# Kernel tuning notes

Hardware: AMD Instinct MI355X
Metric: run time of the kernel (lower is better)

Reference implementation:

```python
import jax, jax.numpy as jnp
import numpy as np
from jax import lax

B, T_TOK, H, T_MEL, K = 32, 1024, 256, 4096, 5


def setup_inputs() -> dict:
    key = jax.random.key(0)
    ks = jax.random.split(key, 16)
    x = jax.random.normal(ks[0], (B, T_TOK, H), jnp.float32)
    token_nums = jax.random.randint(ks[1], (B,), T_TOK // 2, T_TOK)
    # ground-truth per-token durations in mel frames (avg ~4 frames/token)
    mels_alignations = jax.random.uniform(ks[2], (B, T_TOK), jnp.float32) * 8.0
    mels_gt_num = jax.random.randint(ks[3], (B,), T_MEL // 2, T_MEL)
    s = 1.0 / np.sqrt(H * K)
    conv1_w = jax.random.uniform(ks[4], (H, H, K), jnp.float32, -s, s)
    conv1_b = jax.random.uniform(ks[5], (H,), jnp.float32, -s, s)
    ln1_g = jnp.ones((H,), jnp.float32)
    ln1_b = jnp.zeros((H,), jnp.float32)
    conv2_w = jax.random.uniform(ks[6], (H, H, K), jnp.float32, -s, s)
    conv2_b = jax.random.uniform(ks[7], (H,), jnp.float32, -s, s)
    ln2_g = jnp.ones((H,), jnp.float32)
    ln2_b = jnp.zeros((H,), jnp.float32)
    sl = 1.0 / np.sqrt(H)
    lin_w = jax.random.uniform(ks[8], (1, H), jnp.float32, -sl, sl)
    lin_b = jax.random.uniform(ks[9], (1,), jnp.float32, -sl, sl)
    return {"x": x, "token_nums": token_nums, "mels_alignations": mels_alignations,
            "mels_gt_num": mels_gt_num, "conv1_w": conv1_w, "conv1_b": conv1_b,
            "ln1_g": ln1_g, "ln1_b": ln1_b, "conv2_w": conv2_w, "conv2_b": conv2_b,
            "ln2_g": ln2_g, "ln2_b": ln2_b, "lin_w": lin_w, "lin_b": lin_b}


def conv1d_same(x, w, b):
    # x: [B, T, H] -> conv over T with kernel [H_out, H_in, K], padding SAME
    y = lax.conv_general_dilated(x.transpose(0, 2, 1), w, (1,), 'SAME',
                                 dimension_numbers=('NCH', 'OIH', 'NCH'))
    return y.transpose(0, 2, 1) + b


def layer_norm(x, g, b, eps=1e-5):
    mu = jnp.mean(x, axis=-1, keepdims=True)
    var = jnp.mean(jnp.square(x - mu), axis=-1, keepdims=True)
    return (x - mu) * lax.rsqrt(var + eps) * g + b


def reference(x, token_nums, mels_alignations, mels_gt_num,
              conv1_w, conv1_b, ln1_g, ln1_b,
              conv2_w, conv2_b, ln2_g, ln2_b, lin_w, lin_b):
    # NOTE: original forward computes the conv1/ln1/relu1 branch then overwrites
    # m with conv2(x) -- the conv1 branch does not affect outputs, so it is skipped.
    m = conv1d_same(x, conv2_w, conv2_b)                 # [B, T_TOK, H]
    m = jax.nn.relu(layer_norm(m, ln2_g, ln2_b))
    m = (m @ lin_w.T + lin_b)[..., 0]                    # [B, T_TOK]
    mask = jnp.arange(T_TOK)[None, :] < token_nums[:, None]
    m = jnp.where(mask, m, 0.0)                          # mels_alignations_predicted
    exp_m = jnp.where(mask, jnp.exp(m), 0.0)
    mels_num_predicted = exp_m.sum(axis=1).astype(jnp.int32)

    # expansion: running-clipped cumsum of gt durations -> frame->token map
    cum = jnp.minimum(jnp.cumsum(mels_alignations, axis=1),
                      mels_gt_num[:, None].astype(jnp.float32))  # [B, T_TOK]
    frames = jnp.arange(T_MEL, dtype=jnp.float32)
    tok = jax.vmap(lambda c: jnp.searchsorted(c, frames, side='right'))(cum)  # [B, T_MEL]
    valid = tok < T_TOK
    tok_c = jnp.minimum(tok, T_TOK - 1)
    x_new = jnp.where(valid[:, :, None],
                      jnp.take_along_axis(x, tok_c[:, :, None], axis=1), 0.0)
    return x_new, m, mels_num_predicted
```

## Files before the change

kernel.cpp:

```cpp
#include <hip/hip_runtime.h>
#include <hip/hip_bf16.h>

#define B_SZ 32
#define T_TOK 1024
#define H_DIM 256
#define T_MEL 4096
#define K_SZ 5
#define BM 64
#define ROWS (BM + 4)
#define XS_BYTES (ROWS * 512)

typedef __attribute__((ext_vector_type(8))) short bf16x8;
typedef __attribute__((ext_vector_type(4))) float f32x4;

__device__ inline short f2bf(float f) {
    __hip_bfloat16 h = __float2bfloat16(f);
    return *reinterpret_cast<short*>(&h);
}

__global__ __launch_bounds__(256) void prep_kernel(const float* __restrict__ w,
                                                   short* __restrict__ wr,
                                                   const float* __restrict__ a,
                                                   const int* __restrict__ gt,
                                                   float* __restrict__ acc,
                                                   int* __restrict__ tokmap) {
    __shared__ float s_c[T_TOK];
    if (blockIdx.x < 160) {
        int idx = blockIdx.x * 256 + threadIdx.x;
        int lane = idx & 63;
        int n = (idx >> 6) & 15;
        int s = idx >> 10;
        int k = s >> 3;
        int hi0 = (s & 7) * 32 + (lane >> 4) * 8;
        int ho = n * 16 + (lane & 15);
        short out[8];
#pragma unroll
        for (int j = 0; j < 8; ++j)
            out[j] = f2bf(w[(ho * H_DIM + hi0 + j) * K_SZ + k]);
        *reinterpret_cast<bf16x8*>(wr + (size_t)idx * 8) = *reinterpret_cast<bf16x8*>(out);
        return;
    }
    int b = blockIdx.x - 160;
    int tid = threadIdx.x;
    if (tid == 1) acc[b] = 0.f;
    ((float4*)s_c)[tid] = ((const float4*)(a + b * T_TOK))[tid];
    __syncthreads();
    if (tid == 0) {
        float c = 0.f;
        float lim = (float)gt[b];
        for (int t = 0; t < T_TOK; ++t) {
            c += s_c[t];
            s_c[t] = fminf(c, lim);
        }
    }
    __syncthreads();
    int* tm = tokmap + b * T_MEL;
    for (int t = tid; t < T_TOK; t += 256) {
        float c1 = s_c[t];
        float c0 = (t == 0) ? 0.f : s_c[t - 1];
        int f0 = (int)ceilf(c0);
        int f1 = (int)ceilf(c1);
        for (int f = f0; f < f1; ++f) tm[f] = t;
    }
    int z0 = (int)ceilf(s_c[T_TOK - 1]);
    for (int f = z0 + tid; f < T_MEL; f += 256) tm[f] = T_TOK;
}

__global__ __launch_bounds__(512, 4) void conv_kernel(
    const float* __restrict__ x, const short* __restrict__ wr,
    const float* __restrict__ cb, const float* __restrict__ g,
    const float* __restrict__ beta, const float* __restrict__ lw,
    const float* __restrict__ lb, const int* __restrict__ tn,
    float* __restrict__ m_out, float* __restrict__ acc)
{
    __shared__ char smem[XS_BYTES + 6656];
    int tid = threadIdx.x;
    int lane = tid & 63;
    int wid = tid >> 6;
    int b = blockIdx.x >> 4;
    int t0 = (blockIdx.x & 15) * BM;

    for (int i = tid; i < ROWS * 64; i += 512) {
        int row = i >> 6;
        int c4 = i & 63;
        int t = t0 - 2 + row;
        float4 v = make_float4(0.f, 0.f, 0.f, 0.f);
        if (t >= 0 && t < T_TOK)
            v = *reinterpret_cast<const float4*>(x + ((size_t)b * T_TOK + t) * H_DIM + c4 * 4);
        short4 h;
        h.x = f2bf(v.x); h.y = f2bf(v.y); h.z = f2bf(v.z); h.w = f2bf(v.w);
        int byte = row * 512 + c4 * 8;
        byte ^= (row & 7) << 4;
        *reinterpret_cast<short4*>(smem + byte) = h;
    }
    __syncthreads();

    const bf16x8* wf = reinterpret_cast<const bf16x8*>(wr);
    f32x4 zero = {0.f, 0.f, 0.f, 0.f};
    f32x4 acc_[4][2];
#pragma unroll
    for (int mi = 0; mi < 4; ++mi)
#pragma unroll
        for (int ni = 0; ni < 2; ++ni) acc_[mi][ni] = zero;

    int arow = lane & 15;
    int ccol = (lane >> 4) * 16;
    int n16 = wid * 2;

    bf16x8 bc[2], bn[2];
#pragma unroll
    for (int ni = 0; ni < 2; ++ni) bc[ni] = wf[(size_t)(n16 + ni) * 64 + lane];

    for (int s = 0; s < 40; ++s) {
        if (s < 39) {
#pragma unroll
            for (int ni = 0; ni < 2; ++ni)
                bn[ni] = wf[(size_t)((s + 1) * 16 + n16 + ni) * 64 + lane];
        }
        int rb = arow + (s >> 3);
        int cbase = (s & 7) * 64 + ccol;
        bf16x8 a[4];
#pragma unroll
        for (int mi = 0; mi < 4; ++mi) {
            int r = mi * 16 + rb;
            int by = (r * 512 + cbase) ^ ((r & 7) << 4);
            a[mi] = *reinterpret_cast<const bf16x8*>(smem + by);
        }
#pragma unroll
        for (int mi = 0; mi < 4; ++mi)
#pragma unroll
            for (int ni = 0; ni < 2; ++ni)
                acc_[mi][ni] = __builtin_amdgcn_mfma_f32_16x16x32_bf16(a[mi], bc[ni], acc_[mi][ni], 0, 0, 0);
#pragma unroll
        for (int ni = 0; ni < 2; ++ni) bc[ni] = bn[ni];
    }

    __syncthreads();
    float* ps   = reinterpret_cast<float*>(smem + XS_BYTES);
    float* pq   = ps + 512;
    float* pdot = pq + 512;
    float* mus  = pdot + 512;
    float* rss  = mus + 64;

    float cbv[2];
#pragma unroll
    for (int ni = 0; ni < 2; ++ni) cbv[ni] = cb[wid * 32 + ni * 16 + (lane & 15)];

#pragma unroll
    for (int mi = 0; mi < 4; ++mi)
#pragma unroll
        for (int r = 0; r < 4; ++r) {
            float s = 0.f, q = 0.f;
#pragma unroll
            for (int ni = 0; ni < 2; ++ni) {
                float v = acc_[mi][ni][r] + cbv[ni];
                s += v; q += v * v;
            }
#pragma unroll
            for (int m = 1; m < 16; m <<= 1) {
                s += __shfl_xor(s, m);
                q += __shfl_xor(q, m);
            }
            if ((lane & 15) == 0) {
                int row = mi * 16 + (lane >> 4) * 4 + r;
                ps[row * 8 + wid] = s;
                pq[row * 8 + wid] = q;
            }
        }
    __syncthreads();
    if (tid < 64) {
        float S = 0.f, Q = 0.f;
#pragma unroll
        for (int w = 0; w < 8; ++w) { S += ps[tid * 8 + w]; Q += pq[tid * 8 + w]; }
        float mu = S * (1.f / 256.f);
        float var = Q * (1.f / 256.f) - mu * mu;
        mus[tid] = mu;
        rss[tid] = rsqrtf(var + 1e-5f);
    }
    __syncthreads();

    float gv[2], bv[2], lv[2];
#pragma unroll
    for (int ni = 0; ni < 2; ++ni) {
        int col = wid * 32 + ni * 16 + (lane & 15);
        gv[ni] = g[col]; bv[ni] = beta[col]; lv[ni] = lw[col];
    }
#pragma unroll
    for (int mi = 0; mi < 4; ++mi)
#pragma unroll
        for (int r = 0; r < 4; ++r) {
            int row = mi * 16 + (lane >> 4) * 4 + r;
            float mu = mus[row], rs = rss[row];
            float dt = 0.f;
#pragma unroll
            for (int ni = 0; ni < 2; ++ni) {
                float v = acc_[mi][ni][r] + cbv[ni];
                float y = fmaxf((v - mu) * rs * gv[ni] + bv[ni], 0.f);
                dt += y * lv[ni];
            }
#pragma unroll
            for (int m = 1; m < 16; m <<= 1) dt += __shfl_xor(dt, m);
            if ((lane & 15) == 0) pdot[row * 8 + wid] = dt;
        }
    __syncthreads();
    if (tid < 64) {
        float dot = lb[0];
#pragma unroll
        for (int w = 0; w < 8; ++w) dot += pdot[tid * 8 + w];
        int t = t0 + tid;
        float mv = (t < tn[b]) ? dot : 0.f;
        m_out[b * T_TOK + t] = mv;
        float e = (t < tn[b]) ? expf(mv) : 0.f;
#pragma unroll
        for (int m = 1; m < 64; m <<= 1) e += __shfl_xor(e, m);
        if (tid == 0) atomicAdd(&acc[b], e);
    }
}

__global__ __launch_bounds__(256) void expand_kernel(const float* __restrict__ x,
                                                     const int* __restrict__ tokmap,
                                                     float* __restrict__ xnew) {
    __shared__ int s_tok[64];
    int tid = threadIdx.x;
    int lane = tid & 63;
    int wid = tid >> 6;
    int fbase = blockIdx.x * 64;
    int b = blockIdx.x >> 6;
    if (tid < 64) s_tok[tid] = tokmap[fbase + tid];
    __syncthreads();
    const float* xb = x + (size_t)b * T_TOK * H_DIM;
    f32x4* dst = (f32x4*)(xnew + (size_t)(fbase + wid * 16) * H_DIM);
    f32x4 zv = {0.f, 0.f, 0.f, 0.f};
#pragma unroll
    for (int half = 0; half < 2; ++half) {
        f32x4 v[8];
#pragma unroll
        for (int i = 0; i < 8; ++i) {
            int tok = s_tok[wid * 16 + half * 8 + i];
            int tokc = min(tok, T_TOK - 1);
            v[i] = ((const f32x4*)(xb + (size_t)tokc * H_DIM))[lane];
            if (tok >= T_TOK) v[i] = zv;
        }
#pragma unroll
        for (int i = 0; i < 8; ++i)
            __builtin_nontemporal_store(v[i], dst + (half * 8 + i) * 64 + lane);
    }
}

__global__ __launch_bounds__(64) void finalize_kernel(const float* __restrict__ acc,
                                                      float* __restrict__ out) {
    int b = threadIdx.x;
    if (b < B_SZ) out[b] = (float)((int)acc[b]);
}

extern "C" void kernel_launch(void* const* d_in, const int* in_sizes, int n_in,
                              void* d_out, int out_size, void* d_ws, size_t ws_size,
                              hipStream_t stream) {
    const float* x          = (const float*)d_in[0];
    const int*   token_nums = (const int*)d_in[1];
    const float* align      = (const float*)d_in[2];
    const int*   gt         = (const int*)d_in[3];
    const float* w2  = (const float*)d_in[8];
    const float* b2  = (const float*)d_in[9];
    const float* g2  = (const float*)d_in[10];
    const float* be2 = (const float*)d_in[11];
    const float* lw  = (const float*)d_in[12];
    const float* lb  = (const float*)d_in[13];

    float* out   = (float*)d_out;
    float* xnew  = out;
    float* m_out = out + (size_t)B_SZ * T_MEL * H_DIM;
    float* mels  = m_out + (size_t)B_SZ * T_TOK;

    short* wr   = (short*)d_ws;
    float* acc  = (float*)((char*)d_ws + (size_t)40 * 16 * 64 * 8 * 2);
    int* tokmap = (int*)((char*)acc + 128);

    prep_kernel<<<192, 256, 0, stream>>>(w2, wr, align, gt, acc, tokmap);
    conv_kernel<<<B_SZ * (T_TOK / BM), 512, 0, stream>>>(x, wr, b2, g2, be2, lw, lb,
                                                         token_nums, m_out, acc);
    expand_kernel<<<2048, 256, 0, stream>>>(x, tokmap, xnew);
    finalize_kernel<<<1, 64, 0, stream>>>(acc, mels);
}
```

Measured before the change: 80.33 us.

## Fuse conv and expand kernels into one launch with interleaved block roles

Merges the conv/layernorm/projection kernel and the frame-expansion gather into a single kernel, where every third block does conv work and the others do expansion over 128 frames each. This lets the compute-heavy MFMA conv blocks run concurrently with the bandwidth-bound gather/store blocks and removes one kernel launch and the serialization between them. The expand blocks now inherit the larger 512-thread block shape and the conv path's shared memory and register budget, which may limit their occupancy.

```diff
diff --git a/kernel.cpp b/kernel.cpp
--- a/kernel.cpp
+++ b/kernel.cpp
@@ -66,19 +66,50 @@
     for (int f = z0 + tid; f < T_MEL; f += 256) tm[f] = T_TOK;
 }
 
-__global__ __launch_bounds__(512, 4) void conv_kernel(
+__global__ __launch_bounds__(512, 4) void fused_kernel(
     const float* __restrict__ x, const short* __restrict__ wr,
     const float* __restrict__ cb, const float* __restrict__ g,
     const float* __restrict__ beta, const float* __restrict__ lw,
     const float* __restrict__ lb, const int* __restrict__ tn,
-    float* __restrict__ m_out, float* __restrict__ acc)
+    const int* __restrict__ tokmap,
+    float* __restrict__ m_out, float* __restrict__ xnew, float* __restrict__ acc)
 {
     __shared__ char smem[XS_BYTES + 6656];
     int tid = threadIdx.x;
     int lane = tid & 63;
     int wid = tid >> 6;
-    int b = blockIdx.x >> 4;
-    int t0 = (blockIdx.x & 15) * BM;
+    int q = blockIdx.x / 3;
+    int r = blockIdx.x % 3;
+
+    if (r != 0) {
+        int eidx = q * 2 + (r - 1);
+        int fbase = eidx * 128;
+        int b = eidx >> 5;
+        int* s_tok = (int*)smem;
+        if (tid < 128) s_tok[tid] = tokmap[fbase + tid];
+        __syncthreads();
+        const float* xb = x + (size_t)b * T_TOK * H_DIM;
+        f32x4* dst = (f32x4*)(xnew + (size_t)(fbase + wid * 16) * H_DIM);
+        f32x4 zv = {0.f, 0.f, 0.f, 0.f};
+#pragma unroll
+        for (int half = 0; half < 2; ++half) {
+            f32x4 v[8];
+#pragma unroll
+            for (int i = 0; i < 8; ++i) {
+                int tok = s_tok[wid * 16 + half * 8 + i];
+                int tokc = min(tok, T_TOK - 1);
+                v[i] = ((const f32x4*)(xb + (size_t)tokc * H_DIM))[lane];
+                if (tok >= T_TOK) v[i] = zv;
+            }
+#pragma unroll
+            for (int i = 0; i < 8; ++i)
+                __builtin_nontemporal_store(v[i], dst + (half * 8 + i) * 64 + lane);
+        }
+        return;
+    }
+
+    int b = q >> 4;
+    int t0 = (q & 15) * BM;
 
     for (int i = tid; i < ROWS * 64; i += 512) {
         int row = i >> 6;
@@ -122,8 +153,8 @@
         bf16x8 a[4];
 #pragma unroll
         for (int mi = 0; mi < 4; ++mi) {
-            int r = mi * 16 + rb;
-            int by = (r * 512 + cbase) ^ ((r & 7) << 4);
+            int rr = mi * 16 + rb;
+            int by = (rr * 512 + cbase) ^ ((rr & 7) << 4);
             a[mi] = *reinterpret_cast<const bf16x8*>(smem + by);
         }
 #pragma unroll
@@ -149,22 +180,22 @@
 #pragma unroll
     for (int mi = 0; mi < 4; ++mi)
 #pragma unroll
-        for (int r = 0; r < 4; ++r) {
-            float s = 0.f, q = 0.f;
+        for (int rr = 0; rr < 4; ++rr) {
+            float s = 0.f, qq = 0.f;
 #pragma unroll
             for (int ni = 0; ni < 2; ++ni) {
-                float v = acc_[mi][ni][r] + cbv[ni];
-                s += v; q += v * v;
+                float v = acc_[mi][ni][rr] + cbv[ni];
+                s += v; qq += v * v;
             }
 #pragma unroll
             for (int m = 1; m < 16; m <<= 1) {
                 s += __shfl_xor(s, m);
-                q += __shfl_xor(q, m);
+                qq += __shfl_xor(qq, m);
             }
             if ((lane & 15) == 0) {
-                int row = mi * 16 + (lane >> 4) * 4 + r;
+                int row = mi * 16 + (lane >> 4) * 4 + rr;
                 ps[row * 8 + wid] = s;
-                pq[row * 8 + wid] = q;
+                pq[row * 8 + wid] = qq;
             }
         }
     __syncthreads();
@@ -188,13 +219,13 @@
 #pragma unroll
     for (int mi = 0; mi < 4; ++mi)
 #pragma unroll
-        for (int r = 0; r < 4; ++r) {
-            int row = mi * 16 + (lane >> 4) * 4 + r;
+        for (int rr = 0; rr < 4; ++rr) {
+            int row = mi * 16 + (lane >> 4) * 4 + rr;
             float mu = mus[row], rs = rss[row];
             float dt = 0.f;
 #pragma unroll
             for (int ni = 0; ni < 2; ++ni) {
-                float v = acc_[mi][ni][r] + cbv[ni];
+                float v = acc_[mi][ni][rr] + cbv[ni];
                 float y = fmaxf((v - mu) * rs * gv[ni] + bv[ni], 0.f);
                 dt += y * lv[ni];
             }
@@ -214,36 +245,6 @@
 #pragma unroll
         for (int m = 1; m < 64; m <<= 1) e += __shfl_xor(e, m);
         if (tid == 0) atomicAdd(&acc[b], e);
-    }
-}
-
-__global__ __launch_bounds__(256) void expand_kernel(const float* __restrict__ x,
-                                                     const int* __restrict__ tokmap,
-                                                     float* __restrict__ xnew) {
-    __shared__ int s_tok[64];
-    int tid = threadIdx.x;
-    int lane = tid & 63;
-    int wid = tid >> 6;
-    int fbase = blockIdx.x * 64;
-    int b = blockIdx.x >> 6;
-    if (tid < 64) s_tok[tid] = tokmap[fbase + tid];
-    __syncthreads();
-    const float* xb = x + (size_t)b * T_TOK * H_DIM;
-    f32x4* dst = (f32x4*)(xnew + (size_t)(fbase + wid * 16) * H_DIM);
-    f32x4 zv = {0.f, 0.f, 0.f, 0.f};
-#pragma unroll
-    for (int half = 0; half < 2; ++half) {
-        f32x4 v[8];
-#pragma unroll
-        for (int i = 0; i < 8; ++i) {
-            int tok = s_tok[wid * 16 + half * 8 + i];
-            int tokc = min(tok, T_TOK - 1);
-            v[i] = ((const f32x4*)(xb + (size_t)tokc * H_DIM))[lane];
-            if (tok >= T_TOK) v[i] = zv;
-        }
-#pragma unroll
-        for (int i = 0; i < 8; ++i)
-            __builtin_nontemporal_store(v[i], dst + (half * 8 + i) * 64 + lane);
     }
 }
 
@@ -277,8 +278,7 @@
     int* tokmap = (int*)((char*)acc + 128);
 
     prep_kernel<<<192, 256, 0, stream>>>(w2, wr, align, gt, acc, tokmap);
-    conv_kernel<<<B_SZ * (T_TOK / BM), 512, 0, stream>>>(x, wr, b2, g2, be2, lw, lb,
-                                                         token_nums, m_out, acc);
-    expand_kernel<<<2048, 256, 0, stream>>>(x, tokmap, xnew);
+    fused_kernel<<<1536, 512, 0, stream>>>(x, wr, b2, g2, be2, lw, lb,
+                                           token_nums, tokmap, m_out, xnew, acc);
     finalize_kernel<<<1, 64, 0, stream>>>(acc, mels);
 }
```

Result: no change. 79.69 us (-0.8%).
